# Optimization experiments

Hardware: AMD Instinct MI355X
Metric: run time of the kernel (lower is better)

Reference implementation:

```python
import jax, jax.numpy as jnp
import numpy as np

B = 16384
K = 30
LAYERS = 3 * K          # 90
V_LEN = 2 * K           # 60
Z_LEN = 8 * K           # 240
IN_LEN = 3 * K + V_LEN  # 150


def setup_inputs() -> dict:
    key = jax.random.key(0)
    ks = jax.random.split(key, 9)
    Hr = jax.random.normal(ks[0], (B, K), dtype=jnp.float32)
    HH = jax.random.normal(ks[1], (B, K, K), dtype=jnp.float32)
    std = 0.01
    W1 = std * jax.random.normal(ks[2], (LAYERS, Z_LEN, IN_LEN), dtype=jnp.float32)
    b1 = std * jax.random.normal(ks[3], (LAYERS, Z_LEN), dtype=jnp.float32)
    W2 = std * jax.random.normal(ks[4], (LAYERS, K, Z_LEN), dtype=jnp.float32)
    b2 = std * jax.random.normal(ks[5], (LAYERS, K), dtype=jnp.float32)
    W3 = std * jax.random.normal(ks[6], (LAYERS, V_LEN, Z_LEN), dtype=jnp.float32)
    b3 = std * jax.random.normal(ks[7], (LAYERS, V_LEN), dtype=jnp.float32)
    kappa = jax.random.uniform(ks[8], (LAYERS,), dtype=jnp.float32)  # torch.rand(1) per layer
    return {"Hr": Hr, "HH": HH, "W1": W1, "b1": b1, "W2": W2, "b2": b2,
            "W3": W3, "b3": b3, "kappa": kappa}


def reference(Hr, HH, W1, b1, W2, b2, W3, b3, kappa):
    b = Hr.shape[0]
    v0 = jnp.zeros((b, V_LEN), dtype=Hr.dtype)
    t0 = jnp.zeros((b, K), dtype=Hr.dtype)
    tt0 = jnp.zeros((b, K), dtype=Hr.dtype)

    def step(carry, params):
        v, t, t_tilde = carry
        w1, bb1, w2, bb2, w3, bb3, kap = params
        tH = jnp.einsum('bk,bkj->bj', t, HH)                  # [B,K]
        concat = jnp.concatenate([Hr, v, t, tH], axis=1)      # [B,150]
        z = jax.nn.relu(concat @ w1.T + bb1)                  # [B,240]
        t_tilde = t_tilde + z @ w2.T + bb2                    # [B,30]
        ak = jnp.abs(kap)
        t_new = -1.0 + jax.nn.relu(t_tilde + kap) / ak - jax.nn.relu(t_tilde - kap) / ak
        v = v + z @ w3.T + bb3                                # [B,60]
        return (v, t_new, t_tilde), t_new

    _, ts = jax.lax.scan(step, (v0, t0, tt0), (W1, b1, W2, b2, W3, b3, kappa))
    return ts  # [LAYERS, B, K] == t[1:] in torch code
```

## Files before the change

### kernel.cpp

```cpp
#include <hip/hip_runtime.h>

typedef unsigned short u16;
typedef float    f32x4  __attribute__((ext_vector_type(4)));
typedef _Float16 f16x8  __attribute__((ext_vector_type(8)));
typedef short    short8 __attribute__((ext_vector_type(8)));

#define BB 16384
#define KK 30
#define NLAYER 90
#define ROWS 32
#define NBLK (BB / ROWS)
#define THREADS 512

#define NT1 16
#define KS1 5
#define NT2 6
#define KS2 8

#define SZ1  (NLAYER * NT1 * KS1 * 512)
#define SZ23 (NLAYER * NT2 * KS2 * 512)
#define WS_NEEDED ((size_t)4 * (SZ1 + SZ23) + (size_t)4 * (NLAYER * 256 + NLAYER * 96))

#define A_STRIDE 168
#define Z_STRIDE 264
#define TO_STRIDE 33

#define MFMA(a, b, c) __builtin_amdgcn_mfma_f32_16x16x32_f16((a), (b), (c), 0, 0, 0)

__device__ __forceinline__ void splitf(float x, u16& hi, u16& lo) {
    _Float16 h = (_Float16)x;
    _Float16 l = (_Float16)(x - (float)h);
    hi = __builtin_bit_cast(u16, h);
    lo = __builtin_bit_cast(u16, l);
}
__device__ __forceinline__ f16x8 ldfrag(const u16* p) {
    return __builtin_bit_cast(f16x8, *(const short8*)p);
}

__global__ void prep(const float* __restrict__ W1, const float* __restrict__ W2,
                     const float* __restrict__ W3, const float* __restrict__ b1,
                     const float* __restrict__ b2, const float* __restrict__ b3,
                     u16* __restrict__ W1Fhi, u16* __restrict__ W1Flo,
                     u16* __restrict__ W23Fhi, u16* __restrict__ W23Flo,
                     float* __restrict__ b1p, float* __restrict__ b23p)
{
    int idx = blockIdx.x * 256 + threadIdx.x;
    if (idx < SZ1) {
        int j = idx & 7, lane = (idx >> 3) & 63;
        int r = idx >> 9, ks = r % 5; r /= 5;
        int nt = r % 16, l = r / 16;
        int k = ks * 32 + (lane >> 4) * 8 + j;
        int n = nt * 16 + (lane & 15);
        float wv = (k < 150 && n < 240) ? W1[((size_t)l * 240 + n) * 150 + k] : 0.f;
        splitf(wv, W1Fhi[idx], W1Flo[idx]);
    }
    if (idx < SZ23) {
        int j = idx & 7, lane = (idx >> 3) & 63;
        int r = idx >> 9, ks = r % 8; r /= 8;
        int nt = r % 6, l = r / 6;
        int k = ks * 32 + (lane >> 4) * 8 + j;
        int n = nt * 16 + (lane & 15);
        float wv = 0.f;
        if (k < 240) {
            if (n < 30)      wv = W2[((size_t)l * 30 + n) * 240 + k];
            else if (n < 90) wv = W3[((size_t)l * 60 + (n - 30)) * 240 + k];
        }
        splitf(wv, W23Fhi[idx], W23Flo[idx]);
    }
    if (idx < NLAYER * 256) {
        int l = idx >> 8, c = idx & 255;
        b1p[idx] = (c < 240) ? b1[l * 240 + c] : 0.f;
    }
    if (idx < NLAYER * 96) {
        int l = idx / 96, c = idx % 96;
        b23p[idx] = (c < 30) ? b2[l * 30 + c] : (c < 90 ? b3[l * 60 + (c - 30)] : 0.f);
    }
}

__global__ __launch_bounds__(THREADS, 4)
void detnet_kernel(const float* __restrict__ Hr, const float* __restrict__ HH,
                   const float* __restrict__ kappa,
                   const u16* __restrict__ W1Fhi, const u16* __restrict__ W1Flo,
                   const u16* __restrict__ W23Fhi, const u16* __restrict__ W23Flo,
                   const float* __restrict__ b1p, const float* __restrict__ b23p,
                   float* __restrict__ out)
{
    __shared__ u16 aT_hi[ROWS][A_STRIDE], aT_lo[ROWS][A_STRIDE];
    __shared__ u16 zT_hi[ROWS][Z_STRIDE], zT_lo[ROWS][Z_STRIDE];
    __shared__ float tOut[ROWS][TO_STRIDE];

    const int tid  = threadIdx.x;
    const int b0   = blockIdx.x * ROWS;
    const int w    = tid >> 6;
    const int lane = tid & 63;
    const int h    = lane >> 4;
    const int q    = lane & 15;

    const int ra = tid >> 4;
    const int sa = tid & 15;
    float2 hreg[KK];
    if (sa < 15) {
        const float* hh = HH + (size_t)(b0 + ra) * (KK * KK) + 2 * sa;
        #pragma unroll
        for (int k = 0; k < KK; ++k) hreg[k] = *(const float2*)(hh + k * KK);
    } else {
        #pragma unroll
        for (int k = 0; k < KK; ++k) hreg[k] = make_float2(0.f, 0.f);
    }

    float st[2][4];
    #pragma unroll
    for (int m = 0; m < 2; ++m)
        #pragma unroll
        for (int r = 0; r < 4; ++r) st[m][r] = 0.f;

    for (int i = tid; i < ROWS * A_STRIDE; i += THREADS) { (&aT_hi[0][0])[i] = 0; (&aT_lo[0][0])[i] = 0; }
    for (int i = tid; i < ROWS * Z_STRIDE; i += THREADS) { (&zT_hi[0][0])[i] = 0; (&zT_lo[0][0])[i] = 0; }
    for (int i = tid; i < ROWS * TO_STRIDE; i += THREADS) (&tOut[0][0])[i] = 0.f;
    __syncthreads();
    for (int i = tid; i < ROWS * KK; i += THREADS) {
        int r = i / KK, k = i - r * KK;
        splitf(Hr[(size_t)(b0 + r) * KK + k], aT_hi[r][k], aT_lo[r][k]);
    }
    __syncthreads();

    for (int l = 0; l < NLAYER; ++l) {
        if (l > 0 && tid < 240) {
            f32x4 o;
            int e = tid * 4;
            #pragma unroll
            for (int i = 0; i < 4; ++i) {
                int ee = e + i, r = ee / 30, k2 = ee - 30 * r;
                o[i] = tOut[r][k2];
            }
            __builtin_nontemporal_store(o, (f32x4*)(out + ((size_t)(l - 1) * BB + b0) * KK + e));
        }

        if (l > 0 && sa < 15) {
            float a0 = 0.f, a1 = 0.f;
            #pragma unroll
            for (int k = 0; k < KK; ++k) {
                float tk = tOut[ra][k];
                a0 += tk * hreg[k].x;
                a1 += tk * hreg[k].y;
            }
            u16 h0, l0, h1, l1;
            splitf(a0, h0, l0); splitf(a1, h1, l1);
            *(unsigned int*)&aT_hi[ra][120 + 2 * sa] = (unsigned int)h0 | ((unsigned int)h1 << 16);
            *(unsigned int*)&aT_lo[ra][120 + 2 * sa] = (unsigned int)l0 | ((unsigned int)l1 << 16);
        }
        __syncthreads();

        {
            f32x4 acc[2][2];
            #pragma unroll
            for (int i = 0; i < 2; ++i) {
                float bi = b1p[l * 256 + (2 * w + i) * 16 + q];
                f32x4 bv = {bi, bi, bi, bi};
                acc[i][0] = bv; acc[i][1] = bv;
            }
            #pragma unroll 2
            for (int ks = 0; ks < KS1; ++ks) {
                f16x8 ah[2], al[2];
                #pragma unroll
                for (int m = 0; m < 2; ++m) {
                    ah[m] = ldfrag(&aT_hi[m * 16 + q][ks * 32 + h * 8]);
                    al[m] = ldfrag(&aT_lo[m * 16 + q][ks * 32 + h * 8]);
                }
                #pragma unroll
                for (int i = 0; i < 2; ++i) {
                    size_t off = ((((size_t)l * NT1 + 2 * w + i) * KS1 + ks) * 64 + lane) * 8;
                    f16x8 bh = ldfrag(W1Fhi + off);
                    f16x8 bl = ldfrag(W1Flo + off);
                    #pragma unroll
                    for (int m = 0; m < 2; ++m) {
                        acc[i][m] = MFMA(ah[m], bh, acc[i][m]);
                        acc[i][m] = MFMA(ah[m], bl, acc[i][m]);
                        acc[i][m] = MFMA(al[m], bh, acc[i][m]);
                    }
                }
            }
            #pragma unroll
            for (int i = 0; i < 2; ++i)
                #pragma unroll
                for (int m = 0; m < 2; ++m) {
                    int col = (2 * w + i) * 16 + q;
                    #pragma unroll
                    for (int reg = 0; reg < 4; ++reg) {
                        int row = m * 16 + 4 * h + reg;
                        float zv = fmaxf(acc[i][m][reg], 0.f);
                        splitf(zv, zT_hi[row][col], zT_lo[row][col]);
                    }
                }
        }
        __syncthreads();

        if (w < 6) {
            const float kap = kappa[l];
            const float inv = 1.0f / fabsf(kap);
            f32x4 acc[2];
            {
                float bi = b23p[l * 96 + w * 16 + q];
                f32x4 bv = {bi, bi, bi, bi};
                acc[0] = bv; acc[1] = bv;
            }
            #pragma unroll 2
            for (int ks = 0; ks < KS2; ++ks) {
                f16x8 ah[2], al[2];
                #pragma unroll
                for (int m = 0; m < 2; ++m) {
                    ah[m] = ldfrag(&zT_hi[m * 16 + q][ks * 32 + h * 8]);
                    al[m] = ldfrag(&zT_lo[m * 16 + q][ks * 32 + h * 8]);
                }
                size_t off = ((((size_t)l * NT2 + w) * KS2 + ks) * 64 + lane) * 8;
                f16x8 bh = ldfrag(W23Fhi + off);
                f16x8 bl = ldfrag(W23Flo + off);
                #pragma unroll
                for (int m = 0; m < 2; ++m) {
                    acc[m] = MFMA(ah[m], bh, acc[m]);
                    acc[m] = MFMA(ah[m], bl, acc[m]);
                    acc[m] = MFMA(al[m], bh, acc[m]);
                }
            }
            const int col = w * 16 + q;
            const bool isT = col < 30;
            const bool isV = (col >= 30) & (col < 90);
            #pragma unroll
            for (int m = 0; m < 2; ++m)
                #pragma unroll
                for (int reg = 0; reg < 4; ++reg) {
                    float s2 = st[m][reg] + acc[m][reg];
                    int row = m * 16 + 4 * h + reg;
                    if (isT) {
                        st[m][reg] = s2;
                        float tn = -1.0f + fmaxf(s2 + kap, 0.f) * inv - fmaxf(s2 - kap, 0.f) * inv;
                        tOut[row][col] = tn;
                        splitf(tn, aT_hi[row][90 + col], aT_lo[row][90 + col]);
                    } else if (isV) {
                        st[m][reg] = s2;
                        splitf(s2, aT_hi[row][col], aT_lo[row][col]);
                    }
                }
        }
        __syncthreads();
    }

    if (tid < 240) {
        f32x4 o;
        int e = tid * 4;
        #pragma unroll
        for (int i = 0; i < 4; ++i) {
            int ee = e + i, r = ee / 30, k2 = ee - 30 * r;
            o[i] = tOut[r][k2];
        }
        __builtin_nontemporal_store(o, (f32x4*)(out + ((size_t)(NLAYER - 1) * BB + b0) * KK + e));
    }
}

extern "C" void kernel_launch(void* const* d_in, const int* in_sizes, int n_in,
                              void* d_out, int out_size, void* d_ws, size_t ws_size,
                              hipStream_t stream) {
    const float* Hr = (const float*)d_in[0];
    const float* HH = (const float*)d_in[1];
    const float* W1 = (const float*)d_in[2];
    const float* b1 = (const float*)d_in[3];
    const float* W2 = (const float*)d_in[4];
    const float* b2 = (const float*)d_in[5];
    const float* W3 = (const float*)d_in[6];
    const float* b3 = (const float*)d_in[7];
    const float* kp = (const float*)d_in[8];
    float* out = (float*)d_out;

    if (ws_size < WS_NEEDED) return;

    u16* W1Fhi  = (u16*)d_ws;
    u16* W1Flo  = W1Fhi + SZ1;
    u16* W23Fhi = W1Flo + SZ1;
    u16* W23Flo = W23Fhi + SZ23;
    float* b1p  = (float*)(W23Flo + SZ23);
    float* b23p = b1p + NLAYER * 256;

    prep<<<dim3((SZ1 + 255) / 256), dim3(256), 0, stream>>>(
        W1, W2, W3, b1, b2, b3, W1Fhi, W1Flo, W23Fhi, W23Flo, b1p, b23p);
    detnet_kernel<<<dim3(NBLK), dim3(THREADS), 0, stream>>>(
        Hr, HH, kp, W1Fhi, W1Flo, W23Fhi, W23Flo, b1p, b23p, out);
}
```

Baseline: 843.2 us.

## Double rows per block to 64 with 1024 threads and remap MFMA tiles

```diff
diff --git a/kernel.cpp b/kernel.cpp
--- a/kernel.cpp
+++ b/kernel.cpp
@@ -8,9 +8,9 @@
 #define BB 16384
 #define KK 30
 #define NLAYER 90
-#define ROWS 32
+#define ROWS 64
 #define NBLK (BB / ROWS)
-#define THREADS 512
+#define THREADS 1024
 
 #define NT1 16
 #define KS1 5
@@ -108,6 +108,8 @@
         for (int k = 0; k < KK; ++k) hreg[k] = make_float2(0.f, 0.f);
     }
 
+    const int cnt = w >> 1;
+    const int cmh = w & 1;
     float st[2][4];
     #pragma unroll
     for (int m = 0; m < 2; ++m)
@@ -125,7 +127,7 @@
     __syncthreads();
 
     for (int l = 0; l < NLAYER; ++l) {
-        if (l > 0 && tid < 240) {
+        if (l > 0 && tid < ROWS * KK / 4) {
             f32x4 o;
             int e = tid * 4;
             #pragma unroll
@@ -152,92 +154,79 @@
         __syncthreads();
 
         {
-            f32x4 acc[2][2];
-            #pragma unroll
-            for (int i = 0; i < 2; ++i) {
-                float bi = b1p[l * 256 + (2 * w + i) * 16 + q];
+            f32x4 acc[4];
+            {
+                float bi = b1p[l * 256 + w * 16 + q];
                 f32x4 bv = {bi, bi, bi, bi};
-                acc[i][0] = bv; acc[i][1] = bv;
+                #pragma unroll
+                for (int m = 0; m < 4; ++m) acc[m] = bv;
             }
             #pragma unroll 2
             for (int ks = 0; ks < KS1; ++ks) {
-                f16x8 ah[2], al[2];
-                #pragma unroll
-                for (int m = 0; m < 2; ++m) {
-                    ah[m] = ldfrag(&aT_hi[m * 16 + q][ks * 32 + h * 8]);
-                    al[m] = ldfrag(&aT_lo[m * 16 + q][ks * 32 + h * 8]);
-                }
-                #pragma unroll
-                for (int i = 0; i < 2; ++i) {
-                    size_t off = ((((size_t)l * NT1 + 2 * w + i) * KS1 + ks) * 64 + lane) * 8;
-                    f16x8 bh = ldfrag(W1Fhi + off);
-                    f16x8 bl = ldfrag(W1Flo + off);
-                    #pragma unroll
-                    for (int m = 0; m < 2; ++m) {
-                        acc[i][m] = MFMA(ah[m], bh, acc[i][m]);
-                        acc[i][m] = MFMA(ah[m], bl, acc[i][m]);
-                        acc[i][m] = MFMA(al[m], bh, acc[i][m]);
-                    }
-                }
-            }
-            #pragma unroll
-            for (int i = 0; i < 2; ++i)
-                #pragma unroll
-                for (int m = 0; m < 2; ++m) {
-                    int col = (2 * w + i) * 16 + q;
-                    #pragma unroll
-                    for (int reg = 0; reg < 4; ++reg) {
-                        int row = m * 16 + 4 * h + reg;
-                        float zv = fmaxf(acc[i][m][reg], 0.f);
-                        splitf(zv, zT_hi[row][col], zT_lo[row][col]);
-                    }
-                }
+                size_t off = ((((size_t)l * NT1 + w) * KS1 + ks) * 64 + lane) * 8;
+                f16x8 bh = ldfrag(W1Fhi + off);
+                f16x8 bl = ldfrag(W1Flo + off);
+                #pragma unroll
+                for (int m = 0; m < 4; ++m) {
+                    f16x8 ah = ldfrag(&aT_hi[m * 16 + q][ks * 32 + h * 8]);
+                    f16x8 al = ldfrag(&aT_lo[m * 16 + q][ks * 32 + h * 8]);
+                    acc[m] = MFMA(ah, bh, acc[m]);
+                    acc[m] = MFMA(ah, bl, acc[m]);
+                    acc[m] = MFMA(al, bh, acc[m]);
+                }
+            }
+            #pragma unroll
+            for (int m = 0; m < 4; ++m) {
+                int col = w * 16 + q;
+                #pragma unroll
+                for (int reg = 0; reg < 4; ++reg) {
+                    int row = m * 16 + 4 * h + reg;
+                    float zv = fmaxf(acc[m][reg], 0.f);
+                    splitf(zv, zT_hi[row][col], zT_lo[row][col]);
+                }
+            }
         }
         __syncthreads();
 
-        if (w < 6) {
+        if (w < 12) {
             const float kap = kappa[l];
             const float inv = 1.0f / fabsf(kap);
             f32x4 acc[2];
             {
-                float bi = b23p[l * 96 + w * 16 + q];
+                float bi = b23p[l * 96 + cnt * 16 + q];
                 f32x4 bv = {bi, bi, bi, bi};
                 acc[0] = bv; acc[1] = bv;
             }
             #pragma unroll 2
             for (int ks = 0; ks < KS2; ++ks) {
-                f16x8 ah[2], al[2];
-                #pragma unroll
-                for (int m = 0; m < 2; ++m) {
-                    ah[m] = ldfrag(&zT_hi[m * 16 + q][ks * 32 + h * 8]);
-                    al[m] = ldfrag(&zT_lo[m * 16 + q][ks * 32 + h * 8]);
-                }
-                size_t off = ((((size_t)l * NT2 + w) * KS2 + ks) * 64 + lane) * 8;
+                size_t off = ((((size_t)l * NT2 + cnt) * KS2 + ks) * 64 + lane) * 8;
                 f16x8 bh = ldfrag(W23Fhi + off);
                 f16x8 bl = ldfrag(W23Flo + off);
                 #pragma unroll
-                for (int m = 0; m < 2; ++m) {
-                    acc[m] = MFMA(ah[m], bh, acc[m]);
-                    acc[m] = MFMA(ah[m], bl, acc[m]);
-                    acc[m] = MFMA(al[m], bh, acc[m]);
-                }
-            }
-            const int col = w * 16 + q;
+                for (int mm = 0; mm < 2; ++mm) {
+                    f16x8 ah = ldfrag(&zT_hi[(cmh * 2 + mm) * 16 + q][ks * 32 + h * 8]);
+                    f16x8 al = ldfrag(&zT_lo[(cmh * 2 + mm) * 16 + q][ks * 32 + h * 8]);
+                    acc[mm] = MFMA(ah, bh, acc[mm]);
+                    acc[mm] = MFMA(ah, bl, acc[mm]);
+                    acc[mm] = MFMA(al, bh, acc[mm]);
+                }
+            }
+            const int col = cnt * 16 + q;
             const bool isT = col < 30;
             const bool isV = (col >= 30) & (col < 90);
             #pragma unroll
-            for (int m = 0; m < 2; ++m)
+            for (int mm = 0; mm < 2; ++mm)
                 #pragma unroll
                 for (int reg = 0; reg < 4; ++reg) {
-                    float s2 = st[m][reg] + acc[m][reg];
-                    int row = m * 16 + 4 * h + reg;
+                    float s2 = st[mm][reg] + acc[mm][reg];
+                    int row = (cmh * 2 + mm) * 16 + 4 * h + reg;
                     if (isT) {
-                        st[m][reg] = s2;
+                        st[mm][reg] = s2;
                         float tn = -1.0f + fmaxf(s2 + kap, 0.f) * inv - fmaxf(s2 - kap, 0.f) * inv;
                         tOut[row][col] = tn;
                         splitf(tn, aT_hi[row][90 + col], aT_lo[row][90 + col]);
                     } else if (isV) {
-                        st[m][reg] = s2;
+                        st[mm][reg] = s2;
                         splitf(s2, aT_hi[row][col], aT_lo[row][col]);
                     }
                 }
@@ -245,7 +234,7 @@
         __syncthreads();
     }
 
-    if (tid < 240) {
+    if (tid < ROWS * KK / 4) {
         f32x4 o;
         int e = tid * 4;
         #pragma unroll
```

New measurement: 759.2 us. -10.0%, faster.

## Double rows per block to 64 and use 32x32 MFMA for second GEMM

Applied to the files above, without the earlier changes.

```diff
diff --git a/kernel.cpp b/kernel.cpp
--- a/kernel.cpp
+++ b/kernel.cpp
@@ -2,20 +2,21 @@
 
 typedef unsigned short u16;
 typedef float    f32x4  __attribute__((ext_vector_type(4)));
+typedef float    f32x16 __attribute__((ext_vector_type(16)));
 typedef _Float16 f16x8  __attribute__((ext_vector_type(8)));
 typedef short    short8 __attribute__((ext_vector_type(8)));
 
 #define BB 16384
 #define KK 30
 #define NLAYER 90
-#define ROWS 32
+#define ROWS 64
 #define NBLK (BB / ROWS)
-#define THREADS 512
+#define THREADS 1024
 
 #define NT1 16
 #define KS1 5
-#define NT2 6
-#define KS2 8
+#define NT2 3
+#define KS2 16
 
 #define SZ1  (NLAYER * NT1 * KS1 * 512)
 #define SZ23 (NLAYER * NT2 * KS2 * 512)
@@ -25,7 +26,8 @@
 #define Z_STRIDE 264
 #define TO_STRIDE 33
 
-#define MFMA(a, b, c) __builtin_amdgcn_mfma_f32_16x16x32_f16((a), (b), (c), 0, 0, 0)
+#define MFMA16(a, b, c) __builtin_amdgcn_mfma_f32_16x16x32_f16((a), (b), (c), 0, 0, 0)
+#define MFMA32(a, b, c) __builtin_amdgcn_mfma_f32_32x32x16_f16((a), (b), (c), 0, 0, 0)
 
 __device__ __forceinline__ void splitf(float x, u16& hi, u16& lo) {
     _Float16 h = (_Float16)x;
@@ -56,10 +58,10 @@
     }
     if (idx < SZ23) {
         int j = idx & 7, lane = (idx >> 3) & 63;
-        int r = idx >> 9, ks = r % 8; r /= 8;
-        int nt = r % 6, l = r / 6;
-        int k = ks * 32 + (lane >> 4) * 8 + j;
-        int n = nt * 16 + (lane & 15);
+        int r = idx >> 9, ks = r % 16; r /= 16;
+        int nt = r % 3, l = r / 3;
+        int k = ks * 16 + (lane >> 5) * 8 + j;
+        int n = nt * 32 + (lane & 31);
         float wv = 0.f;
         if (k < 240) {
             if (n < 30)      wv = W2[((size_t)l * 30 + n) * 240 + k];
@@ -96,6 +98,14 @@
     const int h    = lane >> 4;
     const int q    = lane & 15;
 
+    const int npair = w & 7;
+    const int mpair = w >> 3;
+
+    const int cnt = w % 3;
+    const int cmt = w / 3;
+    const int e31 = lane & 31;
+    const int e2  = lane >> 5;
+
     const int ra = tid >> 4;
     const int sa = tid & 15;
     float2 hreg[KK];
@@ -108,11 +118,9 @@
         for (int k = 0; k < KK; ++k) hreg[k] = make_float2(0.f, 0.f);
     }
 
-    float st[2][4];
+    f32x16 st;
     #pragma unroll
-    for (int m = 0; m < 2; ++m)
-        #pragma unroll
-        for (int r = 0; r < 4; ++r) st[m][r] = 0.f;
+    for (int r = 0; r < 16; ++r) st[r] = 0.f;
 
     for (int i = tid; i < ROWS * A_STRIDE; i += THREADS) { (&aT_hi[0][0])[i] = 0; (&aT_lo[0][0])[i] = 0; }
     for (int i = tid; i < ROWS * Z_STRIDE; i += THREADS) { (&zT_hi[0][0])[i] = 0; (&zT_lo[0][0])[i] = 0; }
@@ -125,7 +133,7 @@
     __syncthreads();
 
     for (int l = 0; l < NLAYER; ++l) {
-        if (l > 0 && tid < 240) {
+        if (l > 0 && tid < ROWS * KK / 4) {
             f32x4 o;
             int e = tid * 4;
             #pragma unroll
@@ -155,7 +163,7 @@
             f32x4 acc[2][2];
             #pragma unroll
             for (int i = 0; i < 2; ++i) {
-                float bi = b1p[l * 256 + (2 * w + i) * 16 + q];
+                float bi = b1p[l * 256 + (2 * npair + i) * 16 + q];
                 f32x4 bv = {bi, bi, bi, bi};
                 acc[i][0] = bv; acc[i][1] = bv;
             }
@@ -164,19 +172,19 @@
                 f16x8 ah[2], al[2];
                 #pragma unroll
                 for (int m = 0; m < 2; ++m) {
-                    ah[m] = ldfrag(&aT_hi[m * 16 + q][ks * 32 + h * 8]);
-                    al[m] = ldfrag(&aT_lo[m * 16 + q][ks * 32 + h * 8]);
+                    ah[m] = ldfrag(&aT_hi[(2 * mpair + m) * 16 + q][ks * 32 + h * 8]);
+                    al[m] = ldfrag(&aT_lo[(2 * mpair + m) * 16 + q][ks * 32 + h * 8]);
                 }
                 #pragma unroll
                 for (int i = 0; i < 2; ++i) {
-                    size_t off = ((((size_t)l * NT1 + 2 * w + i) * KS1 + ks) * 64 + lane) * 8;
+                    size_t off = ((((size_t)l * NT1 + 2 * npair + i) * KS1 + ks) * 64 + lane) * 8;
                     f16x8 bh = ldfrag(W1Fhi + off);
                     f16x8 bl = ldfrag(W1Flo + off);
                     #pragma unroll
                     for (int m = 0; m < 2; ++m) {
-                        acc[i][m] = MFMA(ah[m], bh, acc[i][m]);
-                        acc[i][m] = MFMA(ah[m], bl, acc[i][m]);
-                        acc[i][m] = MFMA(al[m], bh, acc[i][m]);
+                        acc[i][m] = MFMA16(ah[m], bh, acc[i][m]);
+                        acc[i][m] = MFMA16(ah[m], bl, acc[i][m]);
+                        acc[i][m] = MFMA16(al[m], bh, acc[i][m]);
                     }
                 }
             }
@@ -184,10 +192,10 @@
             for (int i = 0; i < 2; ++i)
                 #pragma unroll
                 for (int m = 0; m < 2; ++m) {
-                    int col = (2 * w + i) * 16 + q;
+                    int col = (2 * npair + i) * 16 + q;
                     #pragma unroll
                     for (int reg = 0; reg < 4; ++reg) {
-                        int row = m * 16 + 4 * h + reg;
+                        int row = (2 * mpair + m) * 16 + 4 * h + reg;
                         float zv = fmaxf(acc[i][m][reg], 0.f);
                         splitf(zv, zT_hi[row][col], zT_lo[row][col]);
                     }
@@ -198,54 +206,45 @@
         if (w < 6) {
             const float kap = kappa[l];
             const float inv = 1.0f / fabsf(kap);
-            f32x4 acc[2];
+            f32x16 acc;
             {
-                float bi = b23p[l * 96 + w * 16 + q];
-                f32x4 bv = {bi, bi, bi, bi};
-                acc[0] = bv; acc[1] = bv;
+                float bi = b23p[l * 96 + cnt * 32 + e31];
+                #pragma unroll
+                for (int r = 0; r < 16; ++r) acc[r] = bi;
             }
             #pragma unroll 2
             for (int ks = 0; ks < KS2; ++ks) {
-                f16x8 ah[2], al[2];
-                #pragma unroll
-                for (int m = 0; m < 2; ++m) {
-                    ah[m] = ldfrag(&zT_hi[m * 16 + q][ks * 32 + h * 8]);
-                    al[m] = ldfrag(&zT_lo[m * 16 + q][ks * 32 + h * 8]);
-                }
-                size_t off = ((((size_t)l * NT2 + w) * KS2 + ks) * 64 + lane) * 8;
+                f16x8 ah = ldfrag(&zT_hi[cmt * 32 + e31][ks * 16 + e2 * 8]);
+                f16x8 al = ldfrag(&zT_lo[cmt * 32 + e31][ks * 16 + e2 * 8]);
+                size_t off = ((((size_t)l * NT2 + cnt) * KS2 + ks) * 64 + lane) * 8;
                 f16x8 bh = ldfrag(W23Fhi + off);
                 f16x8 bl = ldfrag(W23Flo + off);
-                #pragma unroll
-                for (int m = 0; m < 2; ++m) {
-                    acc[m] = MFMA(ah[m], bh, acc[m]);
-                    acc[m] = MFMA(ah[m], bl, acc[m]);
-                    acc[m] = MFMA(al[m], bh, acc[m]);
-                }
-            }
-            const int col = w * 16 + q;
+                acc = MFMA32(ah, bh, acc);
+                acc = MFMA32(ah, bl, acc);
+                acc = MFMA32(al, bh, acc);
+            }
+            const int col = cnt * 32 + e31;
             const bool isT = col < 30;
             const bool isV = (col >= 30) & (col < 90);
             #pragma unroll
-            for (int m = 0; m < 2; ++m)
-                #pragma unroll
-                for (int reg = 0; reg < 4; ++reg) {
-                    float s2 = st[m][reg] + acc[m][reg];
-                    int row = m * 16 + 4 * h + reg;
-                    if (isT) {
-                        st[m][reg] = s2;
-                        float tn = -1.0f + fmaxf(s2 + kap, 0.f) * inv - fmaxf(s2 - kap, 0.f) * inv;
-                        tOut[row][col] = tn;
-                        splitf(tn, aT_hi[row][90 + col], aT_lo[row][90 + col]);
-                    } else if (isV) {
-                        st[m][reg] = s2;
-                        splitf(s2, aT_hi[row][col], aT_lo[row][col]);
-                    }
-                }
+            for (int reg = 0; reg < 16; ++reg) {
+                float s2 = st[reg] + acc[reg];
+                int row = cmt * 32 + (reg & 3) + 8 * (reg >> 2) + 4 * e2;
+                if (isT) {
+                    st[reg] = s2;
+                    float tn = -1.0f + fmaxf(s2 + kap, 0.f) * inv - fmaxf(s2 - kap, 0.f) * inv;
+                    tOut[row][col] = tn;
+                    splitf(tn, aT_hi[row][90 + col], aT_lo[row][90 + col]);
+                } else if (isV) {
+                    st[reg] = s2;
+                    splitf(s2, aT_hi[row][col], aT_lo[row][col]);
+                }
+            }
         }
         __syncthreads();
     }
 
-    if (tid < 240) {
+    if (tid < ROWS * KK / 4) {
         f32x4 o;
         int e = tid * 4;
         #pragma unroll
```

Result: slower. 1.194 ms (+41.5%).
